# Kernel tuning notes

Measured on AMD Instinct MI355X. Metric: run time of the kernel, lower is better.

Reference implementation:

```python
import jax, jax.numpy as jnp
import numpy as np

N_HEAD = 16
D = 1024
LV = 2048
HEAD_DIM = D // N_HEAD
B = 2
LQ = 2048
LN_EPS = 1e-5


def setup_inputs() -> dict:
    key = jax.random.key(0)
    ks = jax.random.split(key, 8)
    s = 0.02
    v = jax.random.normal(ks[0], (B, LV, D), dtype=jnp.float32)
    q = jax.random.normal(ks[1], (B, LQ, D), dtype=jnp.float32)
    # per-head attn linear: d -> lv
    Wa = jax.random.normal(ks[2], (N_HEAD, D, LV), dtype=jnp.float32) * s
    ba = jnp.zeros((N_HEAD, LV), dtype=jnp.float32)
    # per-head layernorm over d
    gamma = jnp.ones((N_HEAD, D), dtype=jnp.float32)
    beta = jnp.zeros((N_HEAD, D), dtype=jnp.float32)
    # per-head proj (FilteredLinear modeled as affine): d -> head_dim
    Wp = jax.random.normal(ks[3], (N_HEAD, D, HEAD_DIM), dtype=jnp.float32) * s
    bp = jnp.zeros((N_HEAD, HEAD_DIM), dtype=jnp.float32)
    return {"v": v, "q": q, "Wa": Wa, "ba": ba, "gamma": gamma,
            "beta": beta, "Wp": Wp, "bp": bp}


def _mha(v, q, Wa, ba, gamma, beta, Wp, bp):
    # attn: [H, B, Lq, Lv] = relu(q @ Wa_h + ba_h)  (batched across heads)
    attn = jax.nn.relu(jnp.einsum('bqd,hdl->hbql', q, Wa)
                       + ba[:, None, None, :])
    # external-attention aggregation: [H, B, Lq, D]
    agg = jnp.einsum('hbql,bld->hbqd', attn, v)
    # per-head LayerNorm over last dim (d)
    mu = jnp.mean(agg, axis=-1, keepdims=True)
    var = jnp.var(agg, axis=-1, keepdims=True)
    normed = (agg - mu) * jax.lax.rsqrt(var + LN_EPS)
    normed = normed * gamma[:, None, None, :] + beta[:, None, None, :]
    # per-head projection to head_dim: [H, B, Lq, head_dim]
    heads = jnp.einsum('hbqd,hde->hbqe', normed, Wp) + bp[:, None, None, :]
    # concat heads along feature dim -> [B, Lq, D]
    return heads.transpose(1, 2, 0, 3).reshape(q.shape[0], q.shape[1], -1)


def reference(v, q, Wa, ba, gamma, beta, Wp, bp):
    return _mha(v, q, Wa, ba, gamma, beta, Wp, bp)
```

## Files before the change

### kernel.cpp

```cpp
#include <hip/hip_runtime.h>
#include <hip/hip_bf16.h>

typedef __attribute__((ext_vector_type(8))) short short8;
typedef __attribute__((ext_vector_type(4))) float f32x4;

#define N_HEAD 16
#define DMODEL 1024
#define LV 2048
#define LQ 2048
#define BATCH 2
#define HEAD_DIM 64

template <int N> struct IC { static constexpr int v = N; };

__device__ inline ushort f2bf(float f) {
    union { float f; unsigned u; } v; v.f = f;
    unsigned r = v.u + 0x7fffu + ((v.u >> 16) & 1u);
    return (ushort)(r >> 16);
}
__device__ inline float bf2f(ushort h) {
    union { unsigned u; float f; } v; v.u = ((unsigned)h) << 16;
    return v.f;
}

__global__ __launch_bounds__(256) void cast_bf16(const float* __restrict__ src,
                                                 ushort* __restrict__ dst, int n) {
    int i = (blockIdx.x * 256 + threadIdx.x) * 4;
    if (i < n) {
        float4 v = *(const float4*)(src + i);
        ushort4 o;
        o.x = f2bf(v.x); o.y = f2bf(v.y); o.z = f2bf(v.z); o.w = f2bf(v.w);
        *(ushort4*)(dst + i) = o;
    }
}

__global__ __launch_bounds__(256) void transpose_cast(const float* __restrict__ src,
                                                      ushort* __restrict__ dst,
                                                      int R, int C) {
    __shared__ float t[32][33];
    size_t zoff = (size_t)blockIdx.z * R * C;
    int c0 = blockIdx.x * 32, r0 = blockIdx.y * 32;
    int tx = threadIdx.x, ty = threadIdx.y;
#pragma unroll
    for (int i = 0; i < 4; ++i)
        t[ty + i * 8][tx] = src[zoff + (size_t)(r0 + ty + i * 8) * C + c0 + tx];
    __syncthreads();
#pragma unroll
    for (int i = 0; i < 4; ++i)
        dst[zoff + (size_t)(c0 + ty + i * 8) * R + r0 + tx] = f2bf(t[tx][ty + i * 8]);
}

template <bool RELU>
__global__ __launch_bounds__(512, 2) void gemm256(
    const ushort* __restrict__ A, const ushort* __restrict__ B,
    ushort* __restrict__ Cout, const float* __restrict__ bias,
    int K,
    long sA_b, long sA_h, long sB_b, long sB_h, long sC_z, int ldc, long sBias_h)
{
    __shared__ __align__(16) char smem[131072];

    const int z = blockIdx.z, b = z & 1, h = z >> 1;
    A += (size_t)b * sA_b + (size_t)h * sA_h;
    B += (size_t)b * sB_b + (size_t)h * sB_h;
    const float* biasp = bias ? bias + (size_t)h * sBias_h : nullptr;

    const int bm0 = blockIdx.y * 256;
    const int bn0 = blockIdx.x * 256;
    const int T = threadIdx.x;
    const int lane = T & 63, wid = T >> 6;
    const int wr = wid >> 2, wc = wid & 3;
    const int fr = lane & 15, fq = lane >> 4;
    const int laneoff = fr * 64 + ((fq * 16) ^ ((fr >> 3) << 5));

    const int s_fr  = (T >> 2) & 15;
    const int s_csw = ((T & 3) * 16) ^ ((s_fr >> 3) << 5);
    const int s_rh  = ((T >> 6) << 4) + s_fr;
    const ushort* gA = A + (size_t)(bm0 + s_rh) * K + (s_csw >> 1);
    const ushort* gB = B + (size_t)(bn0 + s_rh) * K + (s_csw >> 1);
    char* smc = smem;

    const int nt = K >> 5;

    auto stage = [&](int op, int half, int kt) {
        const ushort* src = (op ? gB : gA) + ((size_t)half * 128) * K + (size_t)kt * 32;
        char* dst = smc + (((kt & 3) * 2 + op) << 14) + (half << 13) + (T << 4);
        __builtin_amdgcn_global_load_lds(
            (const __attribute__((address_space(1))) void*)src,
            (__attribute__((address_space(3))) void*)dst, 16, 0, 0);
    };
    auto stage4 = [&](int kt) {
        stage(0, 0, kt); stage(0, 1, kt); stage(1, 0, kt); stage(1, 1, kt);
    };

    struct Frags { short8 a[8]; short8 bb[4]; };
    auto ldfrag = [&](int t, Frags& F) {
        const char* sA = smc + (((t & 3) * 2 + 0) << 14) + wr * 8192 + laneoff;
        const char* sB = smc + (((t & 3) * 2 + 1) << 14) + wc * 4096 + laneoff;
#pragma unroll
        for (int m = 0; m < 8; ++m) F.a[m] = *(const short8*)(sA + m * 1024);
#pragma unroll
        for (int n = 0; n < 4; ++n) F.bb[n] = *(const short8*)(sB + n * 1024);
    };

    f32x4 acc[8][4];
#pragma unroll
    for (int m = 0; m < 8; ++m)
#pragma unroll
        for (int n = 0; n < 4; ++n)
#pragma unroll
            for (int j = 0; j < 4; ++j) acc[m][n][j] = 0.f;

    auto mfma32 = [&](Frags& F) {
        __builtin_amdgcn_s_setprio(1);
#pragma unroll
        for (int m = 0; m < 8; ++m)
#pragma unroll
            for (int n = 0; n < 4; ++n)
                acc[m][n] = __builtin_amdgcn_mfma_f32_16x16x32_bf16(
                    F.a[m], F.bb[n], acc[m][n], 0, 0, 0);
        __builtin_amdgcn_s_setprio(0);
    };

    auto step = [&](int t, Frags& rd, Frags& mm, auto VM, auto DOSTAGE, auto DOREAD) {
        constexpr int vm = decltype(VM)::v;
        if constexpr (decltype(DOREAD)::v)  ldfrag(t + 1, rd);
        if constexpr (decltype(DOSTAGE)::v) stage4(t + 3);
        mfma32(mm);
        __builtin_amdgcn_sched_barrier(0);
        if constexpr (vm == 4)
            asm volatile("s_waitcnt vmcnt(4) lgkmcnt(12)" ::: "memory");
        else if constexpr (vm == 0)
            asm volatile("s_waitcnt vmcnt(0) lgkmcnt(12)" ::: "memory");
        else
            asm volatile("s_waitcnt lgkmcnt(12)" ::: "memory");
        asm volatile("s_barrier" ::: "memory");
    };

    stage4(0); stage4(1); stage4(2);
    asm volatile("s_waitcnt vmcnt(4)" ::: "memory");
    asm volatile("s_barrier" ::: "memory");
    Frags fA, fB;
    ldfrag(0, fA);

    for (int t = 0; t < nt - 4; t += 2) {
        step(t,     fB, fA, IC<4>{}, IC<1>{}, IC<1>{});
        step(t + 1, fA, fB, IC<4>{}, IC<1>{}, IC<1>{});
    }
    step(nt - 4, fB, fA, IC<4>{},  IC<1>{}, IC<1>{});
    step(nt - 3, fA, fB, IC<0>{},  IC<0>{}, IC<1>{});
    step(nt - 2, fB, fA, IC<-1>{}, IC<0>{}, IC<1>{});
    step(nt - 1, fA, fB, IC<-1>{}, IC<0>{}, IC<0>{});

    ushort* C = Cout + (size_t)z * sC_z;
    const int row0 = bm0 + wr * 128;
    const int col0 = bn0 + wc * 64;
#pragma unroll
    for (int n = 0; n < 4; ++n) {
        const int c = col0 + n * 16 + fr;
        const float bvv = biasp ? biasp[c] : 0.f;
#pragma unroll
        for (int m = 0; m < 8; ++m) {
            const int r = row0 + m * 16 + fq * 4;
#pragma unroll
            for (int j = 0; j < 4; ++j) {
                float val = acc[m][n][j] + bvv;
                if (RELU) val = fmaxf(val, 0.f);
                C[(size_t)(r + j) * ldc + c] = f2bf(val);
            }
        }
    }
}

__global__ __launch_bounds__(256) void ln_kernel(ushort* __restrict__ agg,
                                                 const float* __restrict__ gamma,
                                                 const float* __restrict__ beta) {
    const int wid = threadIdx.x >> 6, lane = threadIdx.x & 63;
    const size_t row = (size_t)blockIdx.x * 4 + wid;
    const int h = (int)(row >> 12);
    ushort* p = agg + row * 1024 + lane * 16;
    short8 r0 = *(const short8*)p;
    short8 r1 = *(const short8*)(p + 8);
    float x[16];
#pragma unroll
    for (int j = 0; j < 8; ++j) { x[j] = bf2f((ushort)r0[j]); x[8 + j] = bf2f((ushort)r1[j]); }
    float s = 0.f, s2 = 0.f;
#pragma unroll
    for (int j = 0; j < 16; ++j) { s += x[j]; s2 += x[j] * x[j]; }
    for (int o = 1; o < 64; o <<= 1) {
        s  += __shfl_xor(s,  o, 64);
        s2 += __shfl_xor(s2, o, 64);
    }
    float mu  = s * (1.0f / 1024.0f);
    float var = s2 * (1.0f / 1024.0f) - mu * mu;
    float rs  = rsqrtf(fmaxf(var, 0.f) + 1e-5f);
    const float* g  = gamma + (size_t)h * 1024 + lane * 16;
    const float* bt = beta  + (size_t)h * 1024 + lane * 16;
    short8 o0, o1;
#pragma unroll
    for (int j = 0; j < 8; ++j) {
        o0[j] = (short)f2bf((x[j]     - mu) * rs * g[j]     + bt[j]);
        o1[j] = (short)f2bf((x[8 + j] - mu) * rs * g[8 + j] + bt[8 + j]);
    }
    *(short8*)p = o0;
    *(short8*)(p + 8) = o1;
}

__global__ __launch_bounds__(256) void proj_kernel(const ushort* __restrict__ normed,
                                                   const ushort* __restrict__ WpT,
                                                   const float* __restrict__ bp,
                                                   float* __restrict__ out,
                                                   int h_base) {
    const int z = blockIdx.y, b = z & 1, h = z >> 1;
    const int hg = h_base + h;
    const int wid = threadIdx.x >> 6, lane = threadIdx.x & 63;
    const int fr = lane & 15, fq = lane >> 4;
    const int m0 = (blockIdx.x * 4 + wid) * 16;

    const ushort* Abase = normed + ((size_t)z * 2048 + m0 + fr) * 1024 + fq * 8;
    const ushort* Bbase = WpT + (size_t)hg * 64 * 1024 + (size_t)fr * 1024 + fq * 8;

    f32x4 acc[4];
#pragma unroll
    for (int n = 0; n < 4; ++n)
#pragma unroll
        for (int j = 0; j < 4; ++j) acc[n][j] = 0.f;

    for (int kt = 0; kt < 32; ++kt) {
        short8 a = *(const short8*)(Abase + kt * 32);
#pragma unroll
        for (int n = 0; n < 4; ++n) {
            short8 bb = *(const short8*)(Bbase + n * 16 * 1024 + kt * 32);
            acc[n] = __builtin_amdgcn_mfma_f32_16x16x32_bf16(a, bb, acc[n], 0, 0, 0);
        }
    }
#pragma unroll
    for (int n = 0; n < 4; ++n) {
        int c = hg * 64 + n * 16 + fr;
        float bvv = bp[hg * 64 + n * 16 + fr];
#pragma unroll
        for (int j = 0; j < 4; ++j)
            out[(size_t)b * 2048 * 1024 + (size_t)(m0 + fq * 4 + j) * 1024 + c] =
                acc[n][j] + bvv;
    }
}

extern "C" void kernel_launch(void* const* d_in, const int* in_sizes, int n_in,
                              void* d_out, int out_size, void* d_ws, size_t ws_size,
                              hipStream_t stream) {
    const float* v     = (const float*)d_in[0];
    const float* q     = (const float*)d_in[1];
    const float* Wa    = (const float*)d_in[2];
    const float* ba    = (const float*)d_in[3];
    const float* gamma = (const float*)d_in[4];
    const float* beta  = (const float*)d_in[5];
    const float* Wp    = (const float*)d_in[6];
    const float* bp    = (const float*)d_in[7];
    float* out = (float*)d_out;

    const size_t MB = 1ull << 20;
    char* ws = (char*)d_ws;
    ushort* qbf = (ushort*)(ws);
    ushort* vT  = (ushort*)(ws + 8 * MB);
    ushort* WpT = (ushort*)(ws + 16 * MB);
    int NH = 1;
    {
        const int cands[5] = {16, 8, 4, 2, 1};
        for (int i = 0; i < 5; ++i) {
            if ((size_t)(18 + 28 * cands[i]) * MB <= ws_size) { NH = cands[i]; break; }
        }
    }
    ushort* WaT_c  = (ushort*)(ws + 18 * MB);
    ushort* attn_c = (ushort*)(ws + (18 + (size_t)4 * NH) * MB);
    ushort* agg_c  = (ushort*)(ws + (18 + (size_t)20 * NH) * MB);

    dim3 tb(32, 8);
    cast_bf16<<<4096, 256, 0, stream>>>(q, qbf, BATCH * LQ * DMODEL);
    transpose_cast<<<dim3(DMODEL / 32, LV / 32, BATCH), tb, 0, stream>>>(v, vT, LV, DMODEL);
    transpose_cast<<<dim3(HEAD_DIM / 32, DMODEL / 32, N_HEAD), tb, 0, stream>>>(Wp, WpT, DMODEL, HEAD_DIM);

    for (int h0 = 0; h0 < N_HEAD; h0 += NH) {
        transpose_cast<<<dim3(LV / 32, DMODEL / 32, NH), tb, 0, stream>>>(
            Wa + (size_t)h0 * DMODEL * LV, WaT_c, DMODEL, LV);

        gemm256<true><<<dim3(LV / 256, LQ / 256, NH * 2), 512, 0, stream>>>(
            qbf, WaT_c, attn_c, ba + (size_t)h0 * LV, DMODEL,
            (long)LQ * DMODEL, 0L,
            0L, (long)LV * DMODEL,
            (long)LQ * LV, LV, (long)LV);

        gemm256<false><<<dim3(DMODEL / 256, LQ / 256, NH * 2), 512, 0, stream>>>(
            attn_c, vT, agg_c, nullptr, LV,
            (long)LQ * LV, (long)2 * LQ * LV,
            (long)DMODEL * LV, 0L,
            (long)LQ * DMODEL, DMODEL, 0L);

        ln_kernel<<<(NH * 2 * LQ) / 4, 256, 0, stream>>>(
            agg_c, gamma + (size_t)h0 * DMODEL, beta + (size_t)h0 * DMODEL);

        proj_kernel<<<dim3(LQ / 64, NH * 2), 256, 0, stream>>>(
            agg_c, WpT, bp, out, h0);
    }
}
```

Measured before the change: 831.3 us.

## Restructure GEMM main loop into double-buffered 64-wide K stages with four-phase interleave

Replaces the 4-deep ring of 32-wide K tiles with two 64 KB buffers, each holding a 64-wide K slice. Every K step is split into four phases that each issue half of the A fragments and a slice of the next stage's global-to-LDS loads, then run 16 MFMAs. The goal is to lower register pressure, since fragments are no longer double buffered, and to spread load issue across the MFMA work. In exchange there are more barriers per K step and shallower prefetch, because only one stage is loaded ahead.

```diff
diff --git a/kernel.cpp b/kernel.cpp
--- a/kernel.cpp
+++ b/kernel.cpp
@@ -72,35 +72,29 @@
     const int fr = lane & 15, fq = lane >> 4;
     const int laneoff = fr * 64 + ((fq * 16) ^ ((fr >> 3) << 5));
 
-    const int s_fr  = (T >> 2) & 15;
-    const int s_csw = ((T & 3) * 16) ^ ((s_fr >> 3) << 5);
-    const int s_rh  = ((T >> 6) << 4) + s_fr;
-    const ushort* gA = A + (size_t)(bm0 + s_rh) * K + (s_csw >> 1);
-    const ushort* gB = B + (size_t)(bn0 + s_rh) * K + (s_csw >> 1);
-    char* smc = smem;
-
-    const int nt = K >> 5;
-
-    auto stage = [&](int op, int half, int kt) {
-        const ushort* src = (op ? gB : gA) + ((size_t)half * 128) * K + (size_t)kt * 32;
-        char* dst = smc + (((kt & 3) * 2 + op) << 14) + (half << 13) + (T << 4);
-        __builtin_amdgcn_global_load_lds(
-            (const __attribute__((address_space(1))) void*)src,
-            (__attribute__((address_space(3))) void*)dst, 16, 0, 0);
+    const char* pA0 = smem + 0     + wr * 8192 + laneoff;
+    const char* pB0 = smem + 32768 + wc * 4096 + laneoff;
+    const char* pA1 = pA0 + 65536;
+    const char* pB1 = pB0 + 65536;
+
+    const int s_row = T >> 2;
+    const int s_csw = ((T & 3) * 16) ^ (((T >> 5) & 1) << 5);
+    const ushort* gA = A + (size_t)(bm0 + s_row) * K + (s_csw >> 1);
+    const ushort* gB = B + (size_t)(bn0 + s_row) * K + (s_csw >> 1);
+
+    const int nt = K >> 6;
+
+    auto stage = [&](int op, int kh, int db, int snext) {
+        const ushort* g = op ? gB : gA;
+        const size_t kbase = (size_t)snext * 64 + kh * 32;
+        char* d = smem + db * 65536 + op * 32768 + kh * 16384 + (T << 4);
+#pragma unroll
+        for (int j = 0; j < 2; ++j) {
+            __builtin_amdgcn_global_load_lds(
+                (const __attribute__((address_space(1))) void*)(g + (size_t)j * 128 * K + kbase),
+                (__attribute__((address_space(3))) void*)(d + j * 8192), 16, 0, 0);
+        }
     };
-    auto stage4 = [&](int kt) {
-        stage(0, 0, kt); stage(0, 1, kt); stage(1, 0, kt); stage(1, 1, kt);
-    };
-
-    struct Frags { short8 a[8]; short8 bb[4]; };
-    auto ldfrag = [&](int t, Frags& F) {
-        const char* sA = smc + (((t & 3) * 2 + 0) << 14) + wr * 8192 + laneoff;
-        const char* sB = smc + (((t & 3) * 2 + 1) << 14) + wc * 4096 + laneoff;
-#pragma unroll
-        for (int m = 0; m < 8; ++m) F.a[m] = *(const short8*)(sA + m * 1024);
-#pragma unroll
-        for (int n = 0; n < 4; ++n) F.bb[n] = *(const short8*)(sB + n * 1024);
-    };
 
     f32x4 acc[8][4];
 #pragma unroll
@@ -110,46 +104,63 @@
 #pragma unroll
             for (int j = 0; j < 4; ++j) acc[m][n][j] = 0.f;
 
-    auto mfma32 = [&](Frags& F) {
+    auto phase = [&](const char* pA, const char* pB, short8* bfr, int s, int db,
+                     auto MH, auto KH, auto RDB, auto DOST, auto SOP, auto SKH, auto VM) {
+        constexpr int mh = decltype(MH)::v, kh = decltype(KH)::v;
+        short8 a[4];
+#pragma unroll
+        for (int i = 0; i < 4; ++i)
+            a[i] = *(const short8*)(pA + kh * 16384 + (mh * 4 + i) * 1024);
+        if constexpr (decltype(RDB)::v) {
+#pragma unroll
+            for (int n = 0; n < 4; ++n)
+                bfr[n] = *(const short8*)(pB + kh * 16384 + n * 1024);
+        }
+        if constexpr (decltype(DOST)::v)
+            stage(decltype(SOP)::v, decltype(SKH)::v, db ^ 1, s + 1);
+        asm volatile("s_barrier" ::: "memory");
+        asm volatile("s_waitcnt lgkmcnt(0)" ::: "memory");
+        __builtin_amdgcn_sched_barrier(0);
         __builtin_amdgcn_s_setprio(1);
 #pragma unroll
-        for (int m = 0; m < 8; ++m)
+        for (int i = 0; i < 4; ++i)
 #pragma unroll
             for (int n = 0; n < 4; ++n)
-                acc[m][n] = __builtin_amdgcn_mfma_f32_16x16x32_bf16(
-                    F.a[m], F.bb[n], acc[m][n], 0, 0, 0);
+                acc[mh * 4 + i][n] = __builtin_amdgcn_mfma_f32_16x16x32_bf16(
+                    a[i], bfr[n], acc[mh * 4 + i][n], 0, 0, 0);
         __builtin_amdgcn_s_setprio(0);
-    };
-
-    auto step = [&](int t, Frags& rd, Frags& mm, auto VM, auto DOSTAGE, auto DOREAD) {
+        __builtin_amdgcn_sched_barrier(0);
         constexpr int vm = decltype(VM)::v;
-        if constexpr (decltype(DOREAD)::v)  ldfrag(t + 1, rd);
-        if constexpr (decltype(DOSTAGE)::v) stage4(t + 3);
-        mfma32(mm);
-        __builtin_amdgcn_sched_barrier(0);
-        if constexpr (vm == 4)
-            asm volatile("s_waitcnt vmcnt(4) lgkmcnt(12)" ::: "memory");
-        else if constexpr (vm == 0)
-            asm volatile("s_waitcnt vmcnt(0) lgkmcnt(12)" ::: "memory");
-        else
-            asm volatile("s_waitcnt lgkmcnt(12)" ::: "memory");
+        if constexpr (vm == 4) asm volatile("s_waitcnt vmcnt(4)" ::: "memory");
+        else if constexpr (vm == 0) asm volatile("s_waitcnt vmcnt(0)" ::: "memory");
         asm volatile("s_barrier" ::: "memory");
     };
 
-    stage4(0); stage4(1); stage4(2);
+    auto step_full = [&](int s, const char* pA, const char* pB, int db) {
+        short8 bfr[4];
+        phase(pA, pB, bfr, s, db, IC<0>{}, IC<0>{}, IC<1>{}, IC<1>{}, IC<0>{}, IC<0>{}, IC<-1>{});
+        phase(pA, pB, bfr, s, db, IC<1>{}, IC<0>{}, IC<0>{}, IC<1>{}, IC<1>{}, IC<0>{}, IC<4>{});
+        phase(pA, pB, bfr, s, db, IC<0>{}, IC<1>{}, IC<1>{}, IC<1>{}, IC<0>{}, IC<1>{}, IC<-1>{});
+        phase(pA, pB, bfr, s, db, IC<1>{}, IC<1>{}, IC<0>{}, IC<1>{}, IC<1>{}, IC<1>{}, IC<4>{});
+    };
+    auto step_last = [&](int s, const char* pA, const char* pB, int db) {
+        short8 bfr[4];
+        phase(pA, pB, bfr, s, db, IC<0>{}, IC<0>{}, IC<1>{}, IC<0>{}, IC<0>{}, IC<0>{}, IC<-1>{});
+        phase(pA, pB, bfr, s, db, IC<1>{}, IC<0>{}, IC<0>{}, IC<0>{}, IC<0>{}, IC<0>{}, IC<0>{});
+        phase(pA, pB, bfr, s, db, IC<0>{}, IC<1>{}, IC<1>{}, IC<0>{}, IC<0>{}, IC<0>{}, IC<-1>{});
+        phase(pA, pB, bfr, s, db, IC<1>{}, IC<1>{}, IC<0>{}, IC<0>{}, IC<0>{}, IC<0>{}, IC<-1>{});
+    };
+
+    stage(0, 0, 0, 0); stage(1, 0, 0, 0); stage(0, 1, 0, 0); stage(1, 1, 0, 0);
     asm volatile("s_waitcnt vmcnt(4)" ::: "memory");
     asm volatile("s_barrier" ::: "memory");
-    Frags fA, fB;
-    ldfrag(0, fA);
-
-    for (int t = 0; t < nt - 4; t += 2) {
-        step(t,     fB, fA, IC<4>{}, IC<1>{}, IC<1>{});
-        step(t + 1, fA, fB, IC<4>{}, IC<1>{}, IC<1>{});
-    }
-    step(nt - 4, fB, fA, IC<4>{},  IC<1>{}, IC<1>{});
-    step(nt - 3, fA, fB, IC<0>{},  IC<0>{}, IC<1>{});
-    step(nt - 2, fB, fA, IC<-1>{}, IC<0>{}, IC<1>{});
-    step(nt - 1, fA, fB, IC<-1>{}, IC<0>{}, IC<0>{});
+
+    for (int s = 0; s < nt - 2; s += 2) {
+        step_full(s,     pA0, pB0, 0);
+        step_full(s + 1, pA1, pB1, 1);
+    }
+    step_full(nt - 2, pA0, pB0, 0);
+    step_last(nt - 1, pA1, pB1, 1);
 
     ushort* C = Cout + (size_t)z * sC_z;
     const int row0 = bm0 + wr * 128;
```

New measurement: 817.0 us. No clear change (-1.7%).
